# Kernel tuning notes

Measured on AMD Instinct MI355X. Metric: run time of the kernel, lower is better.

The kernel has to match this reference:

```python
import jax, jax.numpy as jnp
import numpy as np
import math

IN_UNITS, OUT_UNITS, M_SIZE = 1152, 32, 4
CH = M_SIZE * M_SIZE  # out_channels = m_size**2
LAMB, LAMB_MULT, N_ITER = 0.01, 1.2, 3
BATCH = 64


def setup_inputs() -> dict:
    key = jax.random.key(0)
    k1, k2, k3, k4, k5 = jax.random.split(key, 5)
    input_a = jax.random.uniform(k1, (BATCH, IN_UNITS), dtype=jnp.float32)
    input_M = jax.random.normal(k2, (BATCH, IN_UNITS, M_SIZE, M_SIZE), dtype=jnp.float32)
    W = jax.random.normal(k3, (IN_UNITS, OUT_UNITS, M_SIZE, M_SIZE), dtype=jnp.float32)
    beta_u = jax.random.normal(k4, (OUT_UNITS,), dtype=jnp.float32)
    beta_a = jax.random.normal(k5, (OUT_UNITS,), dtype=jnp.float32)
    return {"input_a": input_a, "input_M": input_M, "W": W, "beta_u": beta_u, "beta_a": beta_a}


def reference(input_a, input_M, W, beta_u, beta_a):
    b = input_M.shape[0]
    # votes: pose matrix of each in-capsule transformed by W per out-capsule
    # [b, in, out, m, m] = input_M[b,i] @ W[i,o]
    v = jnp.einsum('bixy,ioyz->bioxz', input_M, W)
    # flatten pose to channels and move in_units last: [b, out, ch, in]
    v_r = v.reshape(b, IN_UNITS, OUT_UNITS, CH).transpose(0, 2, 3, 1)
    # routing assignments R: [b, out, in]
    R = jnp.full((b, OUT_UNITS, IN_UNITS), 1.0 / OUT_UNITS, dtype=jnp.float32)
    a = None
    mu = None
    for it in range(N_ITER):
        R = R * input_a[:, None, :]            # [b, out, in]
        Re = R[:, :, None, :]                  # [b, out, 1, in]
        sum_R = jnp.sum(Re, axis=3)            # [b, out, 1]
        mu = jnp.sum(Re * v_r, axis=3) / sum_R # [b, out, ch]
        diff = v_r - mu[..., None]             # [b, out, ch, in]
        var = jnp.sum(Re * diff * diff, axis=3) / sum_R  # [b, out, ch]
        sigma = jnp.sqrt(var)
        cost = (beta_u[None, :, None] + jnp.log(sigma)) * sum_R  # [b, out, ch]
        lamb = LAMB * LAMB_MULT ** it
        a = jax.nn.sigmoid(lamb * (beta_a[None, :] - jnp.sum(cost, axis=2)))  # [b, out]
        exponent = -jnp.sum(diff * diff / (2.0 * var[..., None]), axis=2)     # [b, out, in]
        eff = jnp.prod(2.0 * math.pi * var, axis=2, keepdims=True)            # [b, out, 1]
        p = eff * jnp.exp(exponent)            # [b, out, in]
        numer = a[..., None] * p               # [b, out, in]
        R = numer / jnp.sum(numer, axis=1, keepdims=True)
    return a, mu
```

## Files before the change

kernel.cpp:

```cpp
#include <hip/hip_runtime.h>
#include <math.h>

#define IN_UNITS 1152
#define OUT_UNITS 32
#define BATCH 64
#define NCHK 24
#define IPB 48
#define NG 6
#define PREC 33
#define PBLK (PREC*OUT_UNITS)

__global__ __launch_bounds__(256) void w_transpose(
    const float* __restrict__ W, float* __restrict__ Wt)
{
    const int gid = blockIdx.x*256 + threadIdx.x;
    const int i = gid >> 9, rem = gid & 511;
    const int y = rem >> 7, o = (rem >> 2) & 31, z = rem & 3;
    Wt[gid] = W[i*512 + o*16 + y*4 + z];
}

template<int MODE>
__global__ __launch_bounds__(256, 4) void caps_main(
    const float* __restrict__ a_in, const float* __restrict__ Mm,
    const float4* __restrict__ Wt4,
    const float* __restrict__ mu_g, const float* __restrict__ i2v_g,
    const float* __restrict__ lae_g,
    float* __restrict__ part)
{
    const int t = threadIdx.x, o = t & 31, il = t >> 5, wv = t >> 6, lane = t & 63;
    const int c = blockIdx.x, b = blockIdx.y, i0 = c*IPB;

    __shared__ float sRed[4][PBLK];

    float rmu[16], ri2[16], lae = 0.f;
    if (MODE) {
        #pragma unroll
        for (int k = 0; k < 16; ++k) {
            rmu[k] = mu_g[b*512 + k*32 + o];
            ri2[k] = i2v_g[b*512 + k*32 + o];
        }
        lae = lae_g[b*32 + o];
    }

    const float4* wbase = Wt4 + (i0 + il)*128 + o;
    const float4* mbase = (const float4*)Mm + (b*IN_UNITS + i0 + il)*4;
    const float*  abase = a_in + b*IN_UNITS + i0 + il;

    float pS = 0.f, pmu[16], pv2[16];
    #pragma unroll
    for (int k = 0; k < 16; ++k) { pmu[k] = 0.f; pv2[k] = 0.f; }

    #pragma unroll
    for (int g = 0; g < NG; ++g) {
        float w[16];
        #pragma unroll
        for (int y = 0; y < 4; ++y) *(float4*)&w[y*4] = wbase[g*1024 + y*32];
        float Mr[16];
        #pragma unroll
        for (int x = 0; x < 4; ++x) *(float4*)&Mr[x*4] = mbase[g*32 + x];
        const float a_val = abase[g*8];

        float v[16];
        #pragma unroll
        for (int x = 0; x < 4; ++x)
            #pragma unroll
            for (int z = 0; z < 4; ++z) {
                float acc = 0.f;
                #pragma unroll
                for (int y = 0; y < 4; ++y)
                    acc = fmaf(Mr[x*4 + y], w[y*4 + z], acc);
                v[x*4 + z] = acc;
            }

        float wgt;
        if (MODE == 0) {
            wgt = a_val * (1.0f/32.0f);
        } else {
            float ex0 = 0.f, ex1 = 0.f;
            #pragma unroll
            for (int k = 0; k < 16; k += 2) {
                float d0 = v[k]   - rmu[k];
                float d1 = v[k+1] - rmu[k+1];
                ex0 = fmaf(d0*d0, ri2[k],   ex0);
                ex1 = fmaf(d1*d1, ri2[k+1], ex1);
            }
            float e = __expf(lae - (ex0 + ex1));
            float s = e;
            #pragma unroll
            for (int m = 16; m >= 1; m >>= 1) s += __shfl_xor(s, m);
            wgt = (e / s) * a_val;
        }

        pS += wgt;
        #pragma unroll
        for (int k = 0; k < 16; ++k) {
            pmu[k] = fmaf(wgt, v[k], pmu[k]);
            pv2[k] = fmaf(wgt*v[k], v[k], pv2[k]);
        }
    }

    pS += __shfl_xor(pS, 32);
    #pragma unroll
    for (int k = 0; k < 16; ++k) {
        pmu[k] += __shfl_xor(pmu[k], 32);
        pv2[k] += __shfl_xor(pv2[k], 32);
    }
    if (lane < 32) {
        float* r = &sRed[wv][0];
        r[o] = pS;
        #pragma unroll
        for (int k = 0; k < 16; ++k) {
            r[(1+k)*32 + o]  = pmu[k];
            r[(17+k)*32 + o] = pv2[k];
        }
    }
    __syncthreads();
    float* dst = part + (b*NCHK + c)*PBLK;
    for (int idx = t; idx < PBLK; idx += 256)
        dst[idx] = sRed[0][idx] + sRed[1][idx] + sRed[2][idx] + sRed[3][idx];
}

__global__ __launch_bounds__(256) void caps_fin(
    const float* __restrict__ part,
    const float* __restrict__ beta_u, const float* __restrict__ beta_a,
    float* __restrict__ mu_g, float* __restrict__ i2v_g, float* __restrict__ lae_g,
    float lamb, float* __restrict__ out)
{
    const int b = blockIdx.x;
    const int t = threadIdx.x;
    const int o = t & 31;
    const int seg = t >> 5;

    float S = 0.f, m[16], q[16];
    #pragma unroll
    for (int k = 0; k < 16; ++k) { m[k] = 0.f; q[k] = 0.f; }
    #pragma unroll
    for (int cc = 0; cc < 3; ++cc) {
        const float* p = part + (b*NCHK + seg + cc*8)*PBLK;
        S += p[o];
        #pragma unroll
        for (int k = 0; k < 16; ++k) {
            m[k] += p[(1+k)*32 + o];
            q[k] += p[(17+k)*32 + o];
        }
    }

    __shared__ float sF[8][PBLK];
    {
        float* r = &sF[seg][0];
        r[o] = S;
        #pragma unroll
        for (int k = 0; k < 16; ++k) { r[(1+k)*32+o] = m[k]; r[(17+k)*32+o] = q[k]; }
    }
    __syncthreads();
    if (t < 32) {
        #pragma unroll
        for (int s = 1; s < 8; ++s) {
            const float* r = &sF[s][0];
            S += r[o];
            #pragma unroll
            for (int k = 0; k < 16; ++k) { m[k] += r[(1+k)*32+o]; q[k] += r[(17+k)*32+o]; }
        }
        const float invS = 1.f / S;
        float mu[16], var[16], logvarsum = 0.f;
        #pragma unroll
        for (int k = 0; k < 16; ++k) {
            mu[k] = m[k] * invS;
            float vv = q[k]*invS - mu[k]*mu[k];
            vv = fmaxf(vv, 1e-30f);
            var[k] = vv;
            logvarsum += logf(vv);
        }
        const float cost = S * (16.f*beta_u[o] + 0.5f*logvarsum);
        const float x = lamb * (beta_a[o] - cost);
        const float log_a = (x >= 0.f) ? -log1pf(expf(-x)) : (x - log1pf(expf(x)));
        const float LOG2PI = 1.8378770664093453f;
        const float logeff = 16.f*LOG2PI + logvarsum;

        const int tid = b*32 + o;
        lae_g[tid] = log_a + logeff;
        #pragma unroll
        for (int k = 0; k < 16; ++k) {
            mu_g[b*512 + k*32 + o]  = mu[k];
            i2v_g[b*512 + k*32 + o] = 0.5f / var[k];
        }
        if (out) {
            out[tid] = 1.f / (1.f + expf(-x));
            #pragma unroll
            for (int k = 0; k < 16; ++k)
                out[BATCH*OUT_UNITS + tid*16 + k] = mu[k];
        }
    }
}

extern "C" void kernel_launch(void* const* d_in, const int* in_sizes, int n_in,
                              void* d_out, int out_size, void* d_ws, size_t ws_size,
                              hipStream_t stream)
{
    const float* a_in = (const float*)d_in[0];
    const float* Mm   = (const float*)d_in[1];
    const float* Wg   = (const float*)d_in[2];
    const float* bu   = (const float*)d_in[3];
    const float* ba   = (const float*)d_in[4];
    float* out = (float*)d_out;

    char* ws = (char*)d_ws;
    size_t off = 0;
    float* part  = (float*)(ws + off); off += (size_t)BATCH*NCHK*PBLK*sizeof(float);
    float* mu_g  = (float*)(ws + off); off += (size_t)BATCH*512*sizeof(float);
    float* i2v_g = (float*)(ws + off); off += (size_t)BATCH*512*sizeof(float);
    float* lae_g = (float*)(ws + off); off += (size_t)BATCH*32*sizeof(float);
    float* Wt    = (float*)(ws + off); off += (size_t)IN_UNITS*OUT_UNITS*16*sizeof(float);

    dim3 grid(NCHK, BATCH), blk(256);
    const float4* Wt4 = (const float4*)Wt;

    w_transpose<<<IN_UNITS*512/256, 256, 0, stream>>>(Wg, Wt);
    caps_main<0><<<grid, blk, 0, stream>>>(a_in, Mm, Wt4, nullptr, nullptr, nullptr, part);
    caps_fin<<<BATCH, 256, 0, stream>>>(part, bu, ba, mu_g, i2v_g, lae_g, 0.01f, nullptr);
    caps_main<1><<<grid, blk, 0, stream>>>(a_in, Mm, Wt4, mu_g, i2v_g, lae_g, part);
    caps_fin<<<BATCH, 256, 0, stream>>>(part, bu, ba, mu_g, i2v_g, lae_g, 0.012f, nullptr);
    caps_main<1><<<grid, blk, 0, stream>>>(a_in, Mm, Wt4, mu_g, i2v_g, lae_g, part);
    caps_fin<<<BATCH, 256, 0, stream>>>(part, bu, ba, mu_g, i2v_g, lae_g, 0.0144f, out);
}
```

Measured before the change: 79.16 us.

## Fuse W transpose into first routing pass and split pose columns across half-waves

Removes the separate W transpose kernel: the first routing pass reads W directly and batch-0 blocks write a float2-interleaved transposed copy that later passes reuse. Each thread now computes only two of the four output columns (8 of 16 pose entries), and the half-wave partial exponents are combined by a shuffle. This halves per-thread register state and drops the cross-half reduction before shared memory, at the cost of twice as many loop iterations per thread and a remapped mu/inv-var layout. It removes one launch, but the first pass now does uncoalesced-ish W reads and extra writes.

```diff
diff --git a/kernel.cpp b/kernel.cpp
--- a/kernel.cpp
+++ b/kernel.cpp
@@ -6,71 +6,76 @@
 #define BATCH 64
 #define NCHK 24
 #define IPB 48
-#define NG 6
+#define NG 12
 #define PREC 33
 #define PBLK (PREC*OUT_UNITS)
 
-__global__ __launch_bounds__(256) void w_transpose(
-    const float* __restrict__ W, float* __restrict__ Wt)
-{
-    const int gid = blockIdx.x*256 + threadIdx.x;
-    const int i = gid >> 9, rem = gid & 511;
-    const int y = rem >> 7, o = (rem >> 2) & 31, z = rem & 3;
-    Wt[gid] = W[i*512 + o*16 + y*4 + z];
+__device__ __forceinline__ int remap16(int k) {
+    return ((k & 2) << 2) + ((k >> 2) << 1) + (k & 1);
 }
 
 template<int MODE>
 __global__ __launch_bounds__(256, 4) void caps_main(
     const float* __restrict__ a_in, const float* __restrict__ Mm,
-    const float4* __restrict__ Wt4,
+    const float* __restrict__ Wg, const float2* __restrict__ Wt2,
+    float2* __restrict__ Wt2w,
     const float* __restrict__ mu_g, const float* __restrict__ i2v_g,
     const float* __restrict__ lae_g,
     float* __restrict__ part)
 {
-    const int t = threadIdx.x, o = t & 31, il = t >> 5, wv = t >> 6, lane = t & 63;
+    const int t = threadIdx.x;
+    const int o = t & 31;
+    const int zh = (t >> 5) & 1;
+    const int wv = t >> 6;
     const int c = blockIdx.x, b = blockIdx.y, i0 = c*IPB;
 
     __shared__ float sRed[4][PBLK];
 
-    float rmu[16], ri2[16], lae = 0.f;
+    float rmu[8], ri2[8], lae = 0.f;
     if (MODE) {
         #pragma unroll
-        for (int k = 0; k < 16; ++k) {
-            rmu[k] = mu_g[b*512 + k*32 + o];
-            ri2[k] = i2v_g[b*512 + k*32 + o];
+        for (int lk = 0; lk < 8; ++lk) {
+            rmu[lk] = mu_g[b*512 + (zh*8 + lk)*32 + o];
+            ri2[lk] = i2v_g[b*512 + (zh*8 + lk)*32 + o];
         }
         lae = lae_g[b*32 + o];
     }
 
-    const float4* wbase = Wt4 + (i0 + il)*128 + o;
-    const float4* mbase = (const float4*)Mm + (b*IN_UNITS + i0 + il)*4;
-    const float*  abase = a_in + b*IN_UNITS + i0 + il;
-
-    float pS = 0.f, pmu[16], pv2[16];
-    #pragma unroll
-    for (int k = 0; k < 16; ++k) { pmu[k] = 0.f; pv2[k] = 0.f; }
+    float pS = 0.f, pmu[8], pv2[8];
+    #pragma unroll
+    for (int lk = 0; lk < 8; ++lk) { pmu[lk] = 0.f; pv2[lk] = 0.f; }
 
     #pragma unroll
     for (int g = 0; g < NG; ++g) {
-        float w[16];
-        #pragma unroll
-        for (int y = 0; y < 4; ++y) *(float4*)&w[y*4] = wbase[g*1024 + y*32];
-        float Mr[16];
-        #pragma unroll
-        for (int x = 0; x < 4; ++x) *(float4*)&Mr[x*4] = mbase[g*32 + x];
-        const float a_val = abase[g*8];
-
-        float v[16];
-        #pragma unroll
-        for (int x = 0; x < 4; ++x)
-            #pragma unroll
-            for (int z = 0; z < 4; ++z) {
-                float acc = 0.f;
+        const int i = i0 + g*4 + wv;
+
+        float2 w2[4];
+        if (MODE == 0) {
+            #pragma unroll
+            for (int y = 0; y < 4; ++y)
+                w2[y] = *(const float2*)(Wg + i*512 + o*16 + y*4 + zh*2);
+            if (b == 0) {
                 #pragma unroll
                 for (int y = 0; y < 4; ++y)
-                    acc = fmaf(Mr[x*4 + y], w[y*4 + z], acc);
-                v[x*4 + z] = acc;
+                    Wt2w[(i*8 + y*2 + zh)*32 + o] = w2[y];
             }
+        } else {
+            #pragma unroll
+            for (int y = 0; y < 4; ++y)
+                w2[y] = Wt2[(i*8 + y*2 + zh)*32 + o];
+        }
+        const float a_val = a_in[b*IN_UNITS + i];
+
+        float v[8];
+        const float4* mrow = (const float4*)(Mm + (b*IN_UNITS + i)*16);
+        #pragma unroll
+        for (int x = 0; x < 4; ++x) {
+            const float4 Mx = mrow[x];
+            v[x*2+0] = fmaf(Mx.x, w2[0].x, fmaf(Mx.y, w2[1].x,
+                       fmaf(Mx.z, w2[2].x, Mx.w*w2[3].x)));
+            v[x*2+1] = fmaf(Mx.x, w2[0].y, fmaf(Mx.y, w2[1].y,
+                       fmaf(Mx.z, w2[2].y, Mx.w*w2[3].y)));
+        }
 
         float wgt;
         if (MODE == 0) {
@@ -78,13 +83,15 @@
         } else {
             float ex0 = 0.f, ex1 = 0.f;
             #pragma unroll
-            for (int k = 0; k < 16; k += 2) {
-                float d0 = v[k]   - rmu[k];
-                float d1 = v[k+1] - rmu[k+1];
-                ex0 = fmaf(d0*d0, ri2[k],   ex0);
-                ex1 = fmaf(d1*d1, ri2[k+1], ex1);
+            for (int lk = 0; lk < 8; lk += 2) {
+                float d0 = v[lk]   - rmu[lk];
+                float d1 = v[lk+1] - rmu[lk+1];
+                ex0 = fmaf(d0*d0, ri2[lk],   ex0);
+                ex1 = fmaf(d1*d1, ri2[lk+1], ex1);
             }
-            float e = __expf(lae - (ex0 + ex1));
+            float exh = ex0 + ex1;
+            float ex = exh + __shfl_xor(exh, 32);
+            float e = __expf(lae - ex);
             float s = e;
             #pragma unroll
             for (int m = 16; m >= 1; m >>= 1) s += __shfl_xor(s, m);
@@ -93,25 +100,20 @@
 
         pS += wgt;
         #pragma unroll
-        for (int k = 0; k < 16; ++k) {
-            pmu[k] = fmaf(wgt, v[k], pmu[k]);
-            pv2[k] = fmaf(wgt*v[k], v[k], pv2[k]);
-        }
-    }
-
-    pS += __shfl_xor(pS, 32);
-    #pragma unroll
-    for (int k = 0; k < 16; ++k) {
-        pmu[k] += __shfl_xor(pmu[k], 32);
-        pv2[k] += __shfl_xor(pv2[k], 32);
-    }
-    if (lane < 32) {
+        for (int lk = 0; lk < 8; ++lk) {
+            pmu[lk] = fmaf(wgt, v[lk], pmu[lk]);
+            pv2[lk] = fmaf(wgt*v[lk], v[lk], pv2[lk]);
+        }
+    }
+
+    {
         float* r = &sRed[wv][0];
-        r[o] = pS;
-        #pragma unroll
-        for (int k = 0; k < 16; ++k) {
-            r[(1+k)*32 + o]  = pmu[k];
-            r[(17+k)*32 + o] = pv2[k];
+        if (zh == 0) r[o] = pS;
+        #pragma unroll
+        for (int lk = 0; lk < 8; ++lk) {
+            const int k = (lk >> 1)*4 + zh*2 + (lk & 1);
+            r[(1+k)*32 + o]  = pmu[lk];
+            r[(17+k)*32 + o] = pv2[lk];
         }
     }
     __syncthreads();
@@ -181,8 +183,8 @@
         lae_g[tid] = log_a + logeff;
         #pragma unroll
         for (int k = 0; k < 16; ++k) {
-            mu_g[b*512 + k*32 + o]  = mu[k];
-            i2v_g[b*512 + k*32 + o] = 0.5f / var[k];
+            mu_g[b*512 + remap16(k)*32 + o]  = mu[k];
+            i2v_g[b*512 + remap16(k)*32 + o] = 0.5f / var[k];
         }
         if (out) {
             out[tid] = 1.f / (1.f + expf(-x));
@@ -213,13 +215,16 @@
     float* Wt    = (float*)(ws + off); off += (size_t)IN_UNITS*OUT_UNITS*16*sizeof(float);
 
     dim3 grid(NCHK, BATCH), blk(256);
-    const float4* Wt4 = (const float4*)Wt;
-
-    w_transpose<<<IN_UNITS*512/256, 256, 0, stream>>>(Wg, Wt);
-    caps_main<0><<<grid, blk, 0, stream>>>(a_in, Mm, Wt4, nullptr, nullptr, nullptr, part);
+    const float2* Wt2 = (const float2*)Wt;
+    float2* Wt2w = (float2*)Wt;
+
+    caps_main<0><<<grid, blk, 0, stream>>>(a_in, Mm, Wg, nullptr, Wt2w,
+                                           nullptr, nullptr, nullptr, part);
     caps_fin<<<BATCH, 256, 0, stream>>>(part, bu, ba, mu_g, i2v_g, lae_g, 0.01f, nullptr);
-    caps_main<1><<<grid, blk, 0, stream>>>(a_in, Mm, Wt4, mu_g, i2v_g, lae_g, part);
+    caps_main<1><<<grid, blk, 0, stream>>>(a_in, Mm, nullptr, Wt2, nullptr,
+                                           mu_g, i2v_g, lae_g, part);
     caps_fin<<<BATCH, 256, 0, stream>>>(part, bu, ba, mu_g, i2v_g, lae_g, 0.012f, nullptr);
-    caps_main<1><<<grid, blk, 0, stream>>>(a_in, Mm, Wt4, mu_g, i2v_g, lae_g, part);
+    caps_main<1><<<grid, blk, 0, stream>>>(a_in, Mm, nullptr, Wt2, nullptr,
+                                           mu_g, i2v_g, lae_g, part);
     caps_fin<<<BATCH, 256, 0, stream>>>(part, bu, ba, mu_g, i2v_g, lae_g, 0.0144f, out);
 }
```

Result: slower. 240.6 us (+204.0%).

## Fuse W transpose into first routing pass and process two batches per block

Applied to the files above, without the earlier changes.

Removes the separate W transpose kernel. The first caps_main pass now reads W in its original layout and one block column writes the transposed copy for later passes. Each block now covers two batch elements with four in-units per group over twelve groups, so the grid has half as many blocks along batch and W loads are shared across two batches within a block. This saves one kernel launch and some W traffic, but it lengthens the per-thread loop and makes the MODE 0 W reads uncoalesced (stride of 16 floats per lane).

```diff
diff --git a/kernel.cpp b/kernel.cpp
--- a/kernel.cpp
+++ b/kernel.cpp
@@ -6,29 +6,24 @@
 #define BATCH 64
 #define NCHK 24
 #define IPB 48
-#define NG 6
+#define NG 12
 #define PREC 33
 #define PBLK (PREC*OUT_UNITS)
-
-__global__ __launch_bounds__(256) void w_transpose(
-    const float* __restrict__ W, float* __restrict__ Wt)
-{
-    const int gid = blockIdx.x*256 + threadIdx.x;
-    const int i = gid >> 9, rem = gid & 511;
-    const int y = rem >> 7, o = (rem >> 2) & 31, z = rem & 3;
-    Wt[gid] = W[i*512 + o*16 + y*4 + z];
-}
 
 template<int MODE>
 __global__ __launch_bounds__(256, 4) void caps_main(
     const float* __restrict__ a_in, const float* __restrict__ Mm,
-    const float4* __restrict__ Wt4,
+    const float* __restrict__ Wg, const float4* __restrict__ Wt4,
+    float4* __restrict__ Wt4w,
     const float* __restrict__ mu_g, const float* __restrict__ i2v_g,
     const float* __restrict__ lae_g,
     float* __restrict__ part)
 {
-    const int t = threadIdx.x, o = t & 31, il = t >> 5, wv = t >> 6, lane = t & 63;
-    const int c = blockIdx.x, b = blockIdx.y, i0 = c*IPB;
+    const int t = threadIdx.x, o = t & 31, il = t >> 5;
+    const int ilq = il & 3, bb = il >> 2, wv = t >> 6, lane = t & 63;
+    const int c = blockIdx.x, bq = blockIdx.y;
+    const int b = bq*2 + bb;
+    const int i0 = c*IPB;
 
     __shared__ float sRed[4][PBLK];
 
@@ -42,9 +37,8 @@
         lae = lae_g[b*32 + o];
     }
 
-    const float4* wbase = Wt4 + (i0 + il)*128 + o;
-    const float4* mbase = (const float4*)Mm + (b*IN_UNITS + i0 + il)*4;
-    const float*  abase = a_in + b*IN_UNITS + i0 + il;
+    const float4* mbase = (const float4*)Mm + (b*IN_UNITS + i0 + ilq)*4;
+    const float*  abase = a_in + b*IN_UNITS + i0 + ilq;
 
     float pS = 0.f, pmu[16], pv2[16];
     #pragma unroll
@@ -52,13 +46,28 @@
 
     #pragma unroll
     for (int g = 0; g < NG; ++g) {
+        const int i = i0 + g*4 + ilq;
+
         float w[16];
-        #pragma unroll
-        for (int y = 0; y < 4; ++y) *(float4*)&w[y*4] = wbase[g*1024 + y*32];
+        if (MODE == 0) {
+            const float4* wp = (const float4*)(Wg + i*512 + o*16);
+            #pragma unroll
+            for (int y = 0; y < 4; ++y) *(float4*)&w[y*4] = wp[y];
+            if (bq == 0 && bb == 0) {
+                #pragma unroll
+                for (int y = 0; y < 4; ++y)
+                    Wt4w[(i*4 + y)*32 + o] = *(const float4*)&w[y*4];
+            }
+        } else {
+            const float4* wp = Wt4 + (i*4)*32 + o;
+            #pragma unroll
+            for (int y = 0; y < 4; ++y) *(float4*)&w[y*4] = wp[y*32];
+        }
+
         float Mr[16];
         #pragma unroll
-        for (int x = 0; x < 4; ++x) *(float4*)&Mr[x*4] = mbase[g*32 + x];
-        const float a_val = abase[g*8];
+        for (int x = 0; x < 4; ++x) *(float4*)&Mr[x*4] = mbase[g*16 + x];
+        const float a_val = abase[g*4];
 
         float v[16];
         #pragma unroll
@@ -115,9 +124,12 @@
         }
     }
     __syncthreads();
-    float* dst = part + (b*NCHK + c)*PBLK;
-    for (int idx = t; idx < PBLK; idx += 256)
-        dst[idx] = sRed[0][idx] + sRed[1][idx] + sRed[2][idx] + sRed[3][idx];
+    float* dst0 = part + ((bq*2 + 0)*NCHK + c)*PBLK;
+    float* dst1 = part + ((bq*2 + 1)*NCHK + c)*PBLK;
+    for (int idx = t; idx < PBLK; idx += 256) {
+        dst0[idx] = sRed[0][idx] + sRed[1][idx];
+        dst1[idx] = sRed[2][idx] + sRed[3][idx];
+    }
 }
 
 __global__ __launch_bounds__(256) void caps_fin(
@@ -162,13 +174,13 @@
             for (int k = 0; k < 16; ++k) { m[k] += r[(1+k)*32+o]; q[k] += r[(17+k)*32+o]; }
         }
         const float invS = 1.f / S;
-        float mu[16], var[16], logvarsum = 0.f;
+        float mu[16], logvarsum = 0.f;
         #pragma unroll
         for (int k = 0; k < 16; ++k) {
             mu[k] = m[k] * invS;
             float vv = q[k]*invS - mu[k]*mu[k];
             vv = fmaxf(vv, 1e-30f);
-            var[k] = vv;
+            q[k] = vv;
             logvarsum += logf(vv);
         }
         const float cost = S * (16.f*beta_u[o] + 0.5f*logvarsum);
@@ -182,7 +194,7 @@
         #pragma unroll
         for (int k = 0; k < 16; ++k) {
             mu_g[b*512 + k*32 + o]  = mu[k];
-            i2v_g[b*512 + k*32 + o] = 0.5f / var[k];
+            i2v_g[b*512 + k*32 + o] = 0.5f / q[k];
         }
         if (out) {
             out[tid] = 1.f / (1.f + expf(-x));
@@ -212,14 +224,17 @@
     float* lae_g = (float*)(ws + off); off += (size_t)BATCH*32*sizeof(float);
     float* Wt    = (float*)(ws + off); off += (size_t)IN_UNITS*OUT_UNITS*16*sizeof(float);
 
-    dim3 grid(NCHK, BATCH), blk(256);
+    dim3 grid(NCHK, BATCH/2), blk(256);
     const float4* Wt4 = (const float4*)Wt;
-
-    w_transpose<<<IN_UNITS*512/256, 256, 0, stream>>>(Wg, Wt);
-    caps_main<0><<<grid, blk, 0, stream>>>(a_in, Mm, Wt4, nullptr, nullptr, nullptr, part);
+    float4* Wt4w = (float4*)Wt;
+
+    caps_main<0><<<grid, blk, 0, stream>>>(a_in, Mm, Wg, nullptr, Wt4w,
+                                           nullptr, nullptr, nullptr, part);
     caps_fin<<<BATCH, 256, 0, stream>>>(part, bu, ba, mu_g, i2v_g, lae_g, 0.01f, nullptr);
-    caps_main<1><<<grid, blk, 0, stream>>>(a_in, Mm, Wt4, mu_g, i2v_g, lae_g, part);
+    caps_main<1><<<grid, blk, 0, stream>>>(a_in, Mm, nullptr, Wt4, nullptr,
+                                           mu_g, i2v_g, lae_g, part);
     caps_fin<<<BATCH, 256, 0, stream>>>(part, bu, ba, mu_g, i2v_g, lae_g, 0.012f, nullptr);
-    caps_main<1><<<grid, blk, 0, stream>>>(a_in, Mm, Wt4, mu_g, i2v_g, lae_g, part);
+    caps_main<1><<<grid, blk, 0, stream>>>(a_in, Mm, nullptr, Wt4, nullptr,
+                                           mu_g, i2v_g, lae_g, part);
     caps_fin<<<BATCH, 256, 0, stream>>>(part, bu, ba, mu_g, i2v_g, lae_g, 0.0144f, out);
 }
```

New measurement: 215.8 us. 2.73x slower.

## Fold W transpose into first finalize kernel and halve per-block chunk size

Applied to the files above, without the earlier changes.

Drops the standalone W transpose launch. The first routing pass now reads W in its original layout with uncoalesced strided float4 loads, and the transpose is done by 64 extra blocks added to the first finalize kernel. Later passes still read the transposed copy. The input dimension is also split into 48 chunks of 24 instead of 24 chunks of 48, which doubles the grid for more parallelism but gives the finalize kernel twice as many partial sums to reduce.

```diff
diff --git a/kernel.cpp b/kernel.cpp
--- a/kernel.cpp
+++ b/kernel.cpp
@@ -4,25 +4,16 @@
 #define IN_UNITS 1152
 #define OUT_UNITS 32
 #define BATCH 64
-#define NCHK 24
-#define IPB 48
-#define NG 6
+#define NCHK 48
+#define IPB 24
+#define NG 3
 #define PREC 33
 #define PBLK (PREC*OUT_UNITS)
-
-__global__ __launch_bounds__(256) void w_transpose(
-    const float* __restrict__ W, float* __restrict__ Wt)
-{
-    const int gid = blockIdx.x*256 + threadIdx.x;
-    const int i = gid >> 9, rem = gid & 511;
-    const int y = rem >> 7, o = (rem >> 2) & 31, z = rem & 3;
-    Wt[gid] = W[i*512 + o*16 + y*4 + z];
-}
 
 template<int MODE>
 __global__ __launch_bounds__(256, 4) void caps_main(
     const float* __restrict__ a_in, const float* __restrict__ Mm,
-    const float4* __restrict__ Wt4,
+    const float* __restrict__ Wg, const float4* __restrict__ Wt4,
     const float* __restrict__ mu_g, const float* __restrict__ i2v_g,
     const float* __restrict__ lae_g,
     float* __restrict__ part)
@@ -42,7 +33,8 @@
         lae = lae_g[b*32 + o];
     }
 
-    const float4* wbase = Wt4 + (i0 + il)*128 + o;
+    const float4* wbase = MODE ? (Wt4 + (i0 + il)*128 + o)
+                               : ((const float4*)Wg + (i0 + il)*128 + o*4);
     const float4* mbase = (const float4*)Mm + (b*IN_UNITS + i0 + il)*4;
     const float*  abase = a_in + b*IN_UNITS + i0 + il;
 
@@ -54,7 +46,8 @@
     for (int g = 0; g < NG; ++g) {
         float w[16];
         #pragma unroll
-        for (int y = 0; y < 4; ++y) *(float4*)&w[y*4] = wbase[g*1024 + y*32];
+        for (int y = 0; y < 4; ++y)
+            *(float4*)&w[y*4] = wbase[g*1024 + (MODE ? y*32 : y)];
         float Mr[16];
         #pragma unroll
         for (int x = 0; x < 4; ++x) *(float4*)&Mr[x*4] = mbase[g*32 + x];
@@ -124,9 +117,21 @@
     const float* __restrict__ part,
     const float* __restrict__ beta_u, const float* __restrict__ beta_a,
     float* __restrict__ mu_g, float* __restrict__ i2v_g, float* __restrict__ lae_g,
-    float lamb, float* __restrict__ out)
+    float lamb, float* __restrict__ out,
+    const float4* __restrict__ Wg4, float4* __restrict__ Wt4)
 {
-    const int b = blockIdx.x;
+    const int bx = blockIdx.x;
+    if (bx >= BATCH) {
+        const int tid = (bx - BATCH)*256 + threadIdx.x;
+        #pragma unroll
+        for (int j = 0; j < 9; ++j) {
+            const int f = j*16384 + tid;
+            const int i = f >> 7, y = (f >> 5) & 3, o = f & 31;
+            Wt4[f] = Wg4[i*128 + o*4 + y];
+        }
+        return;
+    }
+    const int b = bx;
     const int t = threadIdx.x;
     const int o = t & 31;
     const int seg = t >> 5;
@@ -135,7 +140,7 @@
     #pragma unroll
     for (int k = 0; k < 16; ++k) { m[k] = 0.f; q[k] = 0.f; }
     #pragma unroll
-    for (int cc = 0; cc < 3; ++cc) {
+    for (int cc = 0; cc < 6; ++cc) {
         const float* p = part + (b*NCHK + seg + cc*8)*PBLK;
         S += p[o];
         #pragma unroll
@@ -162,13 +167,13 @@
             for (int k = 0; k < 16; ++k) { m[k] += r[(1+k)*32+o]; q[k] += r[(17+k)*32+o]; }
         }
         const float invS = 1.f / S;
-        float mu[16], var[16], logvarsum = 0.f;
+        float mu[16], logvarsum = 0.f;
         #pragma unroll
         for (int k = 0; k < 16; ++k) {
             mu[k] = m[k] * invS;
             float vv = q[k]*invS - mu[k]*mu[k];
             vv = fmaxf(vv, 1e-30f);
-            var[k] = vv;
+            q[k] = vv;
             logvarsum += logf(vv);
         }
         const float cost = S * (16.f*beta_u[o] + 0.5f*logvarsum);
@@ -182,7 +187,7 @@
         #pragma unroll
         for (int k = 0; k < 16; ++k) {
             mu_g[b*512 + k*32 + o]  = mu[k];
-            i2v_g[b*512 + k*32 + o] = 0.5f / var[k];
+            i2v_g[b*512 + k*32 + o] = 0.5f / q[k];
         }
         if (out) {
             out[tid] = 1.f / (1.f + expf(-x));
@@ -214,12 +219,18 @@
 
     dim3 grid(NCHK, BATCH), blk(256);
     const float4* Wt4 = (const float4*)Wt;
-
-    w_transpose<<<IN_UNITS*512/256, 256, 0, stream>>>(Wg, Wt);
-    caps_main<0><<<grid, blk, 0, stream>>>(a_in, Mm, Wt4, nullptr, nullptr, nullptr, part);
-    caps_fin<<<BATCH, 256, 0, stream>>>(part, bu, ba, mu_g, i2v_g, lae_g, 0.01f, nullptr);
-    caps_main<1><<<grid, blk, 0, stream>>>(a_in, Mm, Wt4, mu_g, i2v_g, lae_g, part);
-    caps_fin<<<BATCH, 256, 0, stream>>>(part, bu, ba, mu_g, i2v_g, lae_g, 0.012f, nullptr);
-    caps_main<1><<<grid, blk, 0, stream>>>(a_in, Mm, Wt4, mu_g, i2v_g, lae_g, part);
-    caps_fin<<<BATCH, 256, 0, stream>>>(part, bu, ba, mu_g, i2v_g, lae_g, 0.0144f, out);
+    const float4* Wg4 = (const float4*)Wg;
+
+    caps_main<0><<<grid, blk, 0, stream>>>(a_in, Mm, Wg, nullptr,
+                                           nullptr, nullptr, nullptr, part);
+    caps_fin<<<128, 256, 0, stream>>>(part, bu, ba, mu_g, i2v_g, lae_g,
+                                      0.01f, nullptr, Wg4, (float4*)Wt);
+    caps_main<1><<<grid, blk, 0, stream>>>(a_in, Mm, nullptr, Wt4,
+                                           mu_g, i2v_g, lae_g, part);
+    caps_fin<<<BATCH, 256, 0, stream>>>(part, bu, ba, mu_g, i2v_g, lae_g,
+                                        0.012f, nullptr, nullptr, nullptr);
+    caps_main<1><<<grid, blk, 0, stream>>>(a_in, Mm, nullptr, Wt4,
+                                           mu_g, i2v_g, lae_g, part);
+    caps_fin<<<BATCH, 256, 0, stream>>>(part, bu, ba, mu_g, i2v_g, lae_g,
+                                        0.0144f, out, nullptr, nullptr);
 }
```

Result: slower. 173.4 us (+119.1%).
